# Optimization experiments

Measured on AMD Instinct MI355X. Metric: run time of the kernel, lower is better.

## Reference

```python
import jax, jax.numpy as jnp
import numpy as np

BATCH, HID, STEPS = 64, 2048, 30

def setup_inputs() -> dict:
    key = jax.random.key(0)
    ks = jax.random.split(key, 7)
    s = 1.0 / np.sqrt(HID)  # pytorch LSTM/Linear init scale
    return {
        "monthly_token": jax.random.normal(ks[0], (BATCH, HID), jnp.float32),
        "steps": STEPS,
        "W_ih": jax.random.uniform(ks[1], (4 * HID, HID), jnp.float32, -s, s),
        "W_hh": jax.random.uniform(ks[2], (4 * HID, HID), jnp.float32, -s, s),
        "b_ih": jax.random.uniform(ks[3], (4 * HID,), jnp.float32, -s, s),
        "b_hh": jax.random.uniform(ks[4], (4 * HID,), jnp.float32, -s, s),
        "W_out": jax.random.uniform(ks[5], (1, HID), jnp.float32, -s, s),
        "b_out": jax.random.uniform(ks[6], (1,), jnp.float32, -s, s),
    }

def reference(monthly_token, steps, W_ih, W_hh, b_ih, b_hh, W_out, b_out):
    H = monthly_token.shape[1]
    h0 = monthly_token                      # (B, H) initial hidden
    c0 = jnp.zeros_like(h0)
    x0 = jnp.zeros_like(h0)                 # first lstm input is zeros

    def step(carry, _):
        h, c, x = carry
        # PyTorch gate order: input, forget, cell(g), output
        gates = x @ W_ih.T + b_ih + h @ W_hh.T + b_hh   # (B, 4H)
        i, f, g, o = jnp.split(gates, 4, axis=-1)
        i = jax.nn.sigmoid(i)
        f = jax.nn.sigmoid(f)
        g = jnp.tanh(g)
        o = jax.nn.sigmoid(o)
        c_new = f * c + i * g
        h_new = o * jnp.tanh(c_new)
        y = h_new @ W_out.T + b_out          # (B, 1) daily value
        # feedback: next input is the lstm output (= h_new for 1-layer LSTM)
        return (h_new, c_new, h_new), y[:, 0]

    _, ys = jax.lax.scan(step, (h0, c0, x0), xs=None, length=steps)
    return ys.T                               # (B, steps)
```

## Files before the change

### kernel.cpp

```cpp
#include <hip/hip_runtime.h>
#include <cmath>


#define HID   2048
#define BATCH 64
#define G4    8192
#define NCU   256
#define HGRP  (HID * BATCH / 8)

typedef __attribute__((ext_vector_type(8))) _Float16 half8;
typedef __attribute__((ext_vector_type(4))) float f32x4;

#define LDS_BYTES 158720

__global__ void k_init(const float* __restrict__ token, const float* __restrict__ bih,
                       const float* __restrict__ bhh, half8* __restrict__ h0p,
                       float* __restrict__ bsum, unsigned* __restrict__ flags) {
    int g = blockIdx.x * 256 + threadIdx.x;
    int l = g & 63, nt = (g >> 6) & 3, kt = g >> 8;
    int n = nt * 16 + (l & 15);
    int k0 = kt * 32 + (l >> 4) * 8;
    const float4* ps = (const float4*)(token + (size_t)n * HID + k0);
    float4 a = ps[0], b = ps[1];
    half8 v;
    v[0]=(_Float16)a.x; v[1]=(_Float16)a.y; v[2]=(_Float16)a.z; v[3]=(_Float16)a.w;
    v[4]=(_Float16)b.x; v[5]=(_Float16)b.y; v[6]=(_Float16)b.z; v[7]=(_Float16)b.w;
    h0p[g] = v;
    if (g < G4) bsum[g] = bih[g] + bhh[g];
    if (g < NCU) flags[g] = 0u;
}

__global__ __launch_bounds__(512, 2)
void k_lstm(const float* __restrict__ wih, const float* __restrict__ whh,
            const float* __restrict__ bsum, const float* __restrict__ wout,
            _Float16* __restrict__ hbuf,
            float* __restrict__ ypart,
            unsigned* __restrict__ flags, int steps) {
    extern __shared__ char smem[];
    half8*     Wlds   = (half8*)smem;
    float*     gates  = (float*)(smem + 131072);
    f32x4*     red4   = (f32x4*)(smem + 139264);
    _Float16*  hstage = (_Float16*)(smem + 155648);
    float*     ybuf   = (float*)(smem + 156672);

    const int tid  = threadIdx.x;
    const int blk  = blockIdx.x;
    const int lane = tid & 63;
    const int w    = tid >> 6;
    const int half = w & 1;
    const int ks   = w >> 1;

    for (int idx = tid; idx < 2 * 64 * 64; idx += 512) {
        int l = idx & 63, kt = (idx >> 6) & 63, m2 = idx >> 12;
        int m = l & 15;
        int gate = m2 * 2 + (m >> 3);
        int row  = gate * HID + blk * 8 + (m & 7);
        int col  = kt * 32 + (l >> 4) * 8;
        const float4* p = (const float4*)(whh + (size_t)row * HID + col);
        float4 a = p[0], b = p[1];
        half8 v;
        v[0]=(_Float16)a.x; v[1]=(_Float16)a.y; v[2]=(_Float16)a.z; v[3]=(_Float16)a.w;
        v[4]=(_Float16)b.x; v[5]=(_Float16)b.y; v[6]=(_Float16)b.z; v[7]=(_Float16)b.w;
        Wlds[idx] = v;
    }

    float bias_r[2][4];
    if (ks == 0) {
        const int q = lane >> 4;
        #pragma unroll
        for (int mt2 = 0; mt2 < 2; ++mt2)
            #pragma unroll
            for (int r = 0; r < 4; ++r) {
                int m16 = q * 4 + r;
                bias_r[mt2][r] = bsum[(mt2 * 2 + (m16 >> 3)) * HID + blk * 8 + (m16 & 7)];
            }
    }
    const float wj = wout[blk * 8 + w];
    float creg = 0.0f;
    __syncthreads();

    for (int t = 0; t < steps; ++t) {
        const half8* hp = (const half8*)(hbuf + (size_t)t * HID * BATCH);
        f32x4 a00 = {0,0,0,0}, a01 = {0,0,0,0}, a10 = {0,0,0,0}, a11 = {0,0,0,0};
        const int ktb = ks * 16;
        #pragma unroll
        for (int kk = 0; kk < 16; ++kk) {
            int kt = ktb + kk;
            half8 av0 = Wlds[(kt) * 64 + lane];
            half8 av1 = Wlds[(64 + kt) * 64 + lane];
            half8 b0  = hp[(kt * 4 + half * 2 + 0) * 64 + lane];
            half8 b1  = hp[(kt * 4 + half * 2 + 1) * 64 + lane];
            a00 = __builtin_amdgcn_mfma_f32_16x16x32_f16(av0, b0, a00, 0, 0, 0);
            a01 = __builtin_amdgcn_mfma_f32_16x16x32_f16(av0, b1, a01, 0, 0, 0);
            a10 = __builtin_amdgcn_mfma_f32_16x16x32_f16(av1, b0, a10, 0, 0, 0);
            a11 = __builtin_amdgcn_mfma_f32_16x16x32_f16(av1, b1, a11, 0, 0, 0);
        }
        if (ks == 1 || ks == 3) {
            int srow = (ks == 3 ? 2 : 0) + half;
            red4[(srow * 4 + 0) * 64 + lane] = a00;
            red4[(srow * 4 + 1) * 64 + lane] = a01;
            red4[(srow * 4 + 2) * 64 + lane] = a10;
            red4[(srow * 4 + 3) * 64 + lane] = a11;
        }
        __syncthreads();
        if (ks == 0 || ks == 2) {
            int srow = (ks == 2 ? 2 : 0) + half;
            a00 += red4[(srow * 4 + 0) * 64 + lane];
            a01 += red4[(srow * 4 + 1) * 64 + lane];
            a10 += red4[(srow * 4 + 2) * 64 + lane];
            a11 += red4[(srow * 4 + 3) * 64 + lane];
        }
        __syncthreads();
        if (ks == 2) {
            red4[(half * 4 + 0) * 64 + lane] = a00;
            red4[(half * 4 + 1) * 64 + lane] = a01;
            red4[(half * 4 + 2) * 64 + lane] = a10;
            red4[(half * 4 + 3) * 64 + lane] = a11;
        }
        __syncthreads();
        if (ks == 0) {
            a00 += red4[(half * 4 + 0) * 64 + lane];
            a01 += red4[(half * 4 + 1) * 64 + lane];
            a10 += red4[(half * 4 + 2) * 64 + lane];
            a11 += red4[(half * 4 + 3) * 64 + lane];
            const int q = lane >> 4, col = lane & 15;
            #pragma unroll
            for (int r = 0; r < 4; ++r) {
                float* g0 = gates + (q * 4 + r) * 64 + (half * 2) * 16 + col;
                float* g1 = gates + (16 + q * 4 + r) * 64 + (half * 2) * 16 + col;
                g0[0]  = a00[r] + bias_r[0][r];
                g0[16] = a01[r] + bias_r[0][r];
                g1[0]  = a10[r] + bias_r[1][r];
                g1[16] = a11[r] + bias_r[1][r];
            }
        }
        __syncthreads();
        {
            const int b = lane;
            float gi = gates[(0  + w) * 64 + b];
            float gf = gates[(8  + w) * 64 + b];
            float gg = gates[(16 + w) * 64 + b];
            float go = gates[(24 + w) * 64 + b];
            float iv = 1.0f / (1.0f + __expf(-gi));
            float fv = 1.0f / (1.0f + __expf(-gf));
            float eg = __expf(2.0f * gg);
            float gv = 1.0f - 2.0f / (eg + 1.0f);
            float ov = 1.0f / (1.0f + __expf(-go));
            creg = fv * creg + iv * gv;
            float ec = __expf(2.0f * creg);
            float th = 1.0f - 2.0f / (ec + 1.0f);
            float hv = ov * th;
            hstage[b * 8 + w] = (_Float16)hv;
            ybuf[w * 64 + b]  = hv * wj;
        }
        __syncthreads();
        if (w == 0) {
            const int b = lane;
            if (t < steps - 1) {
                const int kt = blk >> 2, quad = blk & 3;
                const int nt = b >> 4, lp = quad * 16 + (b & 15);
                const size_t g = (size_t)(kt * 4 + nt) * 64 + lp;
                unsigned long long* dst = (unsigned long long*)
                    (hbuf + (size_t)(t + 1) * HID * BATCH + g * 8);
                const unsigned long long* src =
                    (const unsigned long long*)(hstage + b * 8);
                unsigned long long v0 = src[0], v1 = src[1];
                __hip_atomic_store(dst,     v0, __ATOMIC_RELAXED, __HIP_MEMORY_SCOPE_AGENT);
                __hip_atomic_store(dst + 1, v1, __ATOMIC_RELAXED, __HIP_MEMORY_SCOPE_AGENT);
                asm volatile("s_waitcnt vmcnt(0)" ::: "memory");
                if (lane == 0)
                    __hip_atomic_store(&flags[blk], (unsigned)(t + 1),
                                       __ATOMIC_RELAXED, __HIP_MEMORY_SCOPE_AGENT);
            }
            float s = ybuf[lane];
            #pragma unroll
            for (int u = 1; u < 8; ++u) s += ybuf[u * 64 + lane];
            ypart[((size_t)t * NCU + blk) * 64 + lane] = s;
        }
        if (t == 0) {
            for (int idx = tid; idx < 2 * 64 * 64; idx += 512) {
                int l = idx & 63, kt = (idx >> 6) & 63, m2 = idx >> 12;
                int m = l & 15;
                int gate = m2 * 2 + (m >> 3);
                int row  = gate * HID + blk * 8 + (m & 7);
                int col  = kt * 32 + (l >> 4) * 8;
                const float4* p = (const float4*)(wih + (size_t)row * HID + col);
                float4 a = p[0], b = p[1];
                half8 v = Wlds[idx];
                v[0] = (_Float16)((float)v[0] + a.x); v[1] = (_Float16)((float)v[1] + a.y);
                v[2] = (_Float16)((float)v[2] + a.z); v[3] = (_Float16)((float)v[3] + a.w);
                v[4] = (_Float16)((float)v[4] + b.x); v[5] = (_Float16)((float)v[5] + b.y);
                v[6] = (_Float16)((float)v[6] + b.z); v[7] = (_Float16)((float)v[7] + b.w);
                Wlds[idx] = v;
            }
            __syncthreads();
        }
        if (t < steps - 1) {
            while (__hip_atomic_load(&flags[ks * 64 + lane], __ATOMIC_RELAXED,
                                     __HIP_MEMORY_SCOPE_AGENT) <= (unsigned)t)
                __builtin_amdgcn_s_sleep(1);
            asm volatile("" ::: "memory");
        }
    }
}

__global__ __launch_bounds__(512)
void k_yout(const float* __restrict__ ypart, const float* __restrict__ bout,
            float* __restrict__ out, int steps) {
    __shared__ float red[8][64];
    int t = blockIdx.x;
    int tid = threadIdx.x;
    int b = tid & 63, ch = tid >> 6;
    const float* p = ypart + (size_t)t * NCU * 64 + b;
    float s = 0.0f;
    #pragma unroll 8
    for (int cu = ch * 32; cu < ch * 32 + 32; ++cu) s += p[(size_t)cu * 64];
    red[ch][b] = s;
    __syncthreads();
    if (tid < 64) {
        float r = bout[0];
        #pragma unroll
        for (int u = 0; u < 8; ++u) r += red[u][tid];
        out[(size_t)tid * steps + t] = r;
    }
}

extern "C" void kernel_launch(void* const* d_in, const int* in_sizes, int n_in,
                              void* d_out, int out_size, void* d_ws, size_t ws_size,
                              hipStream_t stream) {
    const float* token = (const float*)d_in[0];
    const float* wih   = (const float*)d_in[2];
    const float* whh   = (const float*)d_in[3];
    const float* bih   = (const float*)d_in[4];
    const float* bhh   = (const float*)d_in[5];
    const float* wout  = (const float*)d_in[6];
    const float* bout  = (const float*)d_in[7];
    float* out = (float*)d_out;
    const int steps = out_size / BATCH;

    char* ws = (char*)d_ws;
    size_t off = 0;
    auto carve = [&](size_t bytes) -> void* {
        void* p = ws + off;
        off = (off + bytes + 255) & ~(size_t)255;
        return p;
    };
    _Float16* hbuf  = (_Float16*)carve((size_t)(steps + 1) * HID * BATCH * 2);
    float*    bsum  = (float*)carve((size_t)G4 * 4);
    float*    ypart = (float*)carve((size_t)steps * NCU * 64 * 4);
    unsigned* flags = (unsigned*)carve(NCU * 4);

    hipFuncSetAttribute(reinterpret_cast<const void*>(&k_lstm),
                        hipFuncAttributeMaxDynamicSharedMemorySize, LDS_BYTES);

    k_init<<<dim3(HGRP / 256), dim3(256), 0, stream>>>(
        token, bih, bhh, (half8*)hbuf, bsum, flags);

    k_lstm<<<dim3(NCU), dim3(512), LDS_BYTES, stream>>>(
        wih, whh, bsum, wout, hbuf, ypart, flags, steps);

    k_yout<<<dim3(steps), dim3(512), 0, stream>>>(ypart, bout, out, steps);
}
```

Baseline: 449.7 us.

## Compute gate activations in registers and split flags per batch half

The gate nonlinearities and cell update now run directly on the MFMA accumulators in the two reducing waves, using lane shuffles instead of staging gates, h and y through LDS. This removes two block barriers per step and folds the two-stage cross-wave reduction into one fewer sync. Flags are split by batch half, so each wave waits only for the producers of the h columns it actually reads, and the wait is moved to the start of the step. The activation work is concentrated on 2 waves instead of 8, and each store now writes 8 bytes per lane.

```diff
diff --git a/kernel.cpp b/kernel.cpp
--- a/kernel.cpp
+++ b/kernel.cpp
@@ -7,11 +7,12 @@
 #define G4    8192
 #define NCU   256
 #define HGRP  (HID * BATCH / 8)
+#define NFLAGS 512
 
 typedef __attribute__((ext_vector_type(8))) _Float16 half8;
 typedef __attribute__((ext_vector_type(4))) float f32x4;
 
-#define LDS_BYTES 158720
+#define LDS_BYTES 155648
 
 __global__ void k_init(const float* __restrict__ token, const float* __restrict__ bih,
                        const float* __restrict__ bhh, half8* __restrict__ h0p,
@@ -27,7 +28,7 @@
     v[4]=(_Float16)b.x; v[5]=(_Float16)b.y; v[6]=(_Float16)b.z; v[7]=(_Float16)b.w;
     h0p[g] = v;
     if (g < G4) bsum[g] = bih[g] + bhh[g];
-    if (g < NCU) flags[g] = 0u;
+    if (g < NFLAGS) flags[g] = 0u;
 }
 
 __global__ __launch_bounds__(512, 2)
@@ -37,11 +38,8 @@
             float* __restrict__ ypart,
             unsigned* __restrict__ flags, int steps) {
     extern __shared__ char smem[];
-    half8*     Wlds   = (half8*)smem;
-    float*     gates  = (float*)(smem + 131072);
-    f32x4*     red4   = (f32x4*)(smem + 139264);
-    _Float16*  hstage = (_Float16*)(smem + 155648);
-    float*     ybuf   = (float*)(smem + 156672);
+    half8* Wlds = (half8*)smem;
+    f32x4* red4 = (f32x4*)(smem + 131072);
 
     const int tid  = threadIdx.x;
     const int blk  = blockIdx.x;
@@ -49,14 +47,16 @@
     const int w    = tid >> 6;
     const int half = w & 1;
     const int ks   = w >> 1;
+    const int q    = lane >> 4;
+    const int col  = lane & 15;
 
     for (int idx = tid; idx < 2 * 64 * 64; idx += 512) {
         int l = idx & 63, kt = (idx >> 6) & 63, m2 = idx >> 12;
         int m = l & 15;
         int gate = m2 * 2 + (m >> 3);
         int row  = gate * HID + blk * 8 + (m & 7);
-        int col  = kt * 32 + (l >> 4) * 8;
-        const float4* p = (const float4*)(whh + (size_t)row * HID + col);
+        int colw = kt * 32 + (l >> 4) * 8;
+        const float4* p = (const float4*)(whh + (size_t)row * HID + colw);
         float4 a = p[0], b = p[1];
         half8 v;
         v[0]=(_Float16)a.x; v[1]=(_Float16)a.y; v[2]=(_Float16)a.z; v[3]=(_Float16)a.w;
@@ -64,22 +64,28 @@
         Wlds[idx] = v;
     }
 
-    float bias_r[2][4];
-    if (ks == 0) {
-        const int q = lane >> 4;
+    float biasA[4] = {0,0,0,0}, biasB[4] = {0,0,0,0}, wj4[4] = {0,0,0,0};
+    float c4[4] = {0.0f, 0.0f, 0.0f, 0.0f};
+    if (w < 2) {
         #pragma unroll
-        for (int mt2 = 0; mt2 < 2; ++mt2)
-            #pragma unroll
-            for (int r = 0; r < 4; ++r) {
-                int m16 = q * 4 + r;
-                bias_r[mt2][r] = bsum[(mt2 * 2 + (m16 >> 3)) * HID + blk * 8 + (m16 & 7)];
-            }
-    }
-    const float wj = wout[blk * 8 + w];
-    float creg = 0.0f;
+        for (int r = 0; r < 4; ++r) {
+            int rA = 4 * q + r;
+            int rB = 16 + 4 * q + r;
+            biasA[r] = bsum[(rA >> 3) * HID + blk * 8 + (rA & 7)];
+            biasB[r] = bsum[(rB >> 3) * HID + blk * 8 + (rB & 7)];
+            wj4[r]   = wout[blk * 8 + (q & 1) * 4 + r];
+        }
+    }
     __syncthreads();
 
     for (int t = 0; t < steps; ++t) {
+        if (t) {
+            while (__hip_atomic_load(&flags[half * NCU + ks * 64 + lane],
+                                     __ATOMIC_RELAXED, __HIP_MEMORY_SCOPE_AGENT)
+                   < (unsigned)t)
+                __builtin_amdgcn_s_sleep(1);
+            asm volatile("" ::: "memory");
+        }
         const half8* hp = (const half8*)(hbuf + (size_t)t * HID * BATCH);
         f32x4 a00 = {0,0,0,0}, a01 = {0,0,0,0}, a10 = {0,0,0,0}, a11 = {0,0,0,0};
         const int ktb = ks * 16;
@@ -103,79 +109,87 @@
             red4[(srow * 4 + 3) * 64 + lane] = a11;
         }
         __syncthreads();
-        if (ks == 0 || ks == 2) {
-            int srow = (ks == 2 ? 2 : 0) + half;
+        if (ks == 0) {
+            int srow = half;
             a00 += red4[(srow * 4 + 0) * 64 + lane];
             a01 += red4[(srow * 4 + 1) * 64 + lane];
             a10 += red4[(srow * 4 + 2) * 64 + lane];
             a11 += red4[(srow * 4 + 3) * 64 + lane];
+        } else if (ks == 2) {
+            int srow = 2 + half;
+            a00 += red4[(srow * 4 + 0) * 64 + lane];
+            a01 += red4[(srow * 4 + 1) * 64 + lane];
+            a10 += red4[(srow * 4 + 2) * 64 + lane];
+            a11 += red4[(srow * 4 + 3) * 64 + lane];
+            int sdst = 4 + half;
+            red4[(sdst * 4 + 0) * 64 + lane] = a00;
+            red4[(sdst * 4 + 1) * 64 + lane] = a01;
+            red4[(sdst * 4 + 2) * 64 + lane] = a10;
+            red4[(sdst * 4 + 3) * 64 + lane] = a11;
         }
         __syncthreads();
-        if (ks == 2) {
-            red4[(half * 4 + 0) * 64 + lane] = a00;
-            red4[(half * 4 + 1) * 64 + lane] = a01;
-            red4[(half * 4 + 2) * 64 + lane] = a10;
-            red4[(half * 4 + 3) * 64 + lane] = a11;
-        }
-        __syncthreads();
-        if (ks == 0) {
-            a00 += red4[(half * 4 + 0) * 64 + lane];
-            a01 += red4[(half * 4 + 1) * 64 + lane];
-            a10 += red4[(half * 4 + 2) * 64 + lane];
-            a11 += red4[(half * 4 + 3) * 64 + lane];
-            const int q = lane >> 4, col = lane & 15;
+        if (w < 2) {
+            int srow = 4 + half;
+            a00 += red4[(srow * 4 + 0) * 64 + lane];
+            a01 += red4[(srow * 4 + 1) * 64 + lane];
+            a10 += red4[(srow * 4 + 2) * 64 + lane];
+            a11 += red4[(srow * 4 + 3) * 64 + lane];
             #pragma unroll
             for (int r = 0; r < 4; ++r) {
-                float* g0 = gates + (q * 4 + r) * 64 + (half * 2) * 16 + col;
-                float* g1 = gates + (16 + q * 4 + r) * 64 + (half * 2) * 16 + col;
-                g0[0]  = a00[r] + bias_r[0][r];
-                g0[16] = a01[r] + bias_r[0][r];
-                g1[0]  = a10[r] + bias_r[1][r];
-                g1[16] = a11[r] + bias_r[1][r];
-            }
-        }
-        __syncthreads();
-        {
-            const int b = lane;
-            float gi = gates[(0  + w) * 64 + b];
-            float gf = gates[(8  + w) * 64 + b];
-            float gg = gates[(16 + w) * 64 + b];
-            float go = gates[(24 + w) * 64 + b];
-            float iv = 1.0f / (1.0f + __expf(-gi));
-            float fv = 1.0f / (1.0f + __expf(-gf));
-            float eg = __expf(2.0f * gg);
-            float gv = 1.0f - 2.0f / (eg + 1.0f);
-            float ov = 1.0f / (1.0f + __expf(-go));
-            creg = fv * creg + iv * gv;
-            float ec = __expf(2.0f * creg);
-            float th = 1.0f - 2.0f / (ec + 1.0f);
-            float hv = ov * th;
-            hstage[b * 8 + w] = (_Float16)hv;
-            ybuf[w * 64 + b]  = hv * wj;
-        }
-        __syncthreads();
-        if (w == 0) {
-            const int b = lane;
+                a00[r] += biasA[r]; a01[r] += biasA[r];
+                a10[r] += biasB[r]; a11[r] += biasB[r];
+            }
+            float x00[4], x01[4], x10[4], x11[4];
+            #pragma unroll
+            for (int r = 0; r < 4; ++r) {
+                x00[r] = __shfl_xor(a00[r], 32);
+                x01[r] = __shfl_xor(a01[r], 32);
+                x10[r] = __shfl_xor(a10[r], 32);
+                x11[r] = __shfl_xor(a11[r], 32);
+            }
+            const bool lo = (lane < 32);
+            float hv[4];
+            #pragma unroll
+            for (int r = 0; r < 4; ++r) {
+                float gi = lo ? a00[r] : x01[r];
+                float gf = lo ? x00[r] : a01[r];
+                float gg = lo ? a10[r] : x11[r];
+                float go = lo ? x10[r] : a11[r];
+                float iv = 1.0f / (1.0f + __expf(-gi));
+                float fv = 1.0f / (1.0f + __expf(-gf));
+                float eg = __expf(2.0f * gg);
+                float gv = 1.0f - 2.0f / (eg + 1.0f);
+                float ov = 1.0f / (1.0f + __expf(-go));
+                c4[r] = fv * c4[r] + iv * gv;
+                float ec = __expf(2.0f * c4[r]);
+                float th = 1.0f - 2.0f / (ec + 1.0f);
+                hv[r] = ov * th;
+            }
             if (t < steps - 1) {
-                const int kt = blk >> 2, quad = blk & 3;
-                const int nt = b >> 4, lp = quad * 16 + (b & 15);
-                const size_t g = (size_t)(kt * 4 + nt) * 64 + lp;
+                union { unsigned short us[4]; unsigned long long ull; } pk;
+                #pragma unroll
+                for (int r = 0; r < 4; ++r) {
+                    _Float16 hf = (_Float16)hv[r];
+                    pk.us[r] = *(unsigned short*)&hf;
+                }
+                const int nt = half * 2 + (q >> 1);
+                const size_t g = (size_t)((blk >> 2) * 4 + nt) * 64
+                               + (blk & 3) * 16 + col;
                 unsigned long long* dst = (unsigned long long*)
-                    (hbuf + (size_t)(t + 1) * HID * BATCH + g * 8);
-                const unsigned long long* src =
-                    (const unsigned long long*)(hstage + b * 8);
-                unsigned long long v0 = src[0], v1 = src[1];
-                __hip_atomic_store(dst,     v0, __ATOMIC_RELAXED, __HIP_MEMORY_SCOPE_AGENT);
-                __hip_atomic_store(dst + 1, v1, __ATOMIC_RELAXED, __HIP_MEMORY_SCOPE_AGENT);
+                    (hbuf + (size_t)(t + 1) * HID * BATCH + g * 8) + (q & 1);
+                __hip_atomic_store(dst, pk.ull, __ATOMIC_RELAXED,
+                                   __HIP_MEMORY_SCOPE_AGENT);
                 asm volatile("s_waitcnt vmcnt(0)" ::: "memory");
                 if (lane == 0)
-                    __hip_atomic_store(&flags[blk], (unsigned)(t + 1),
+                    __hip_atomic_store(&flags[half * NCU + blk], (unsigned)(t + 1),
                                        __ATOMIC_RELAXED, __HIP_MEMORY_SCOPE_AGENT);
             }
-            float s = ybuf[lane];
-            #pragma unroll
-            for (int u = 1; u < 8; ++u) s += ybuf[u * 64 + lane];
-            ypart[((size_t)t * NCU + blk) * 64 + lane] = s;
+            float yp = wj4[0] * hv[0] + wj4[1] * hv[1]
+                     + wj4[2] * hv[2] + wj4[3] * hv[3];
+            yp += __shfl_xor(yp, 16);
+            if ((q & 1) == 0)
+                ypart[((size_t)t * NCU + blk) * 64
+                      + half * 32 + (q >> 1) * 16 + col] = yp;
         }
         if (t == 0) {
             for (int idx = tid; idx < 2 * 64 * 64; idx += 512) {
@@ -183,8 +197,8 @@
                 int m = l & 15;
                 int gate = m2 * 2 + (m >> 3);
                 int row  = gate * HID + blk * 8 + (m & 7);
-                int col  = kt * 32 + (l >> 4) * 8;
-                const float4* p = (const float4*)(wih + (size_t)row * HID + col);
+                int colw = kt * 32 + (l >> 4) * 8;
+                const float4* p = (const float4*)(wih + (size_t)row * HID + colw);
                 float4 a = p[0], b = p[1];
                 half8 v = Wlds[idx];
                 v[0] = (_Float16)((float)v[0] + a.x); v[1] = (_Float16)((float)v[1] + a.y);
@@ -194,12 +208,6 @@
                 Wlds[idx] = v;
             }
             __syncthreads();
-        }
-        if (t < steps - 1) {
-            while (__hip_atomic_load(&flags[ks * 64 + lane], __ATOMIC_RELAXED,
-                                     __HIP_MEMORY_SCOPE_AGENT) <= (unsigned)t)
-                __builtin_amdgcn_s_sleep(1);
-            asm volatile("" ::: "memory");
         }
     }
 }
@@ -248,7 +256,7 @@
     _Float16* hbuf  = (_Float16*)carve((size_t)(steps + 1) * HID * BATCH * 2);
     float*    bsum  = (float*)carve((size_t)G4 * 4);
     float*    ypart = (float*)carve((size_t)steps * NCU * 64 * 4);
-    unsigned* flags = (unsigned*)carve(NCU * 4);
+    unsigned* flags = (unsigned*)carve(NFLAGS * 4);
 
     hipFuncSetAttribute(reinterpret_cast<const void*>(&k_lstm),
                         hipFuncAttributeMaxDynamicSharedMemorySize, LDS_BYTES);
```

After: 457.0 us. About the same (+1.6%).
